# Kernel tuning notes

Hardware: AMD Instinct MI355X
Metric: run time of the kernel (lower is better)

## Reference

```python
import jax, jax.numpy as jnp
import numpy as np

N = 50000  # num nodes


def _gcn_layer(x, W, b, src, dst, dinv):
    # PyG GCNConv: transform first, then normalized neighbor aggregation
    h = x @ W                                   # [N, out]
    norm = dinv[src] * dinv[dst]                # [E]
    msg = h[src] * norm[:, None]                # gather + scale, [E, out]
    agg = jax.ops.segment_sum(msg, dst, num_segments=N)
    agg = agg + h * (dinv * dinv)[:, None]      # self-loop term (weight 1)
    return agg + b


def setup_inputs() -> dict:
    key = jax.random.key(0)
    ks = jax.random.split(key, 9)
    x = jax.random.normal(ks[0], (N, 256), dtype=jnp.float32)
    edge_index = jax.random.randint(ks[1], (2, 800000), 0, N, dtype=jnp.int64)
    def lin(kw, kb, fan_in, fan_out):
        s = 1.0 / np.sqrt(fan_in)
        W = jax.random.uniform(kw, (fan_in, fan_out), jnp.float32, -s, s)
        b = jax.random.uniform(kb, (fan_out,), jnp.float32, -s, s)
        return W, b
    W0, b0 = lin(ks[2], ks[3], 256, 128)
    W1, b1 = lin(ks[4], ks[5], 128, 128)
    W2, b2 = lin(ks[6], ks[7], 128, 64)
    return {"x": x, "edge_index": edge_index,
            "W0": W0, "b0": b0, "W1": W1, "b1": b1, "W2": W2, "b2": b2}


def reference(x, edge_index, W0, b0, W1, b1, W2, b2):
    src, dst = edge_index[0], edge_index[1]
    # degree with implicit self loops (edge weights = 1)
    deg = jax.ops.segment_sum(jnp.ones_like(dst, dtype=x.dtype), dst,
                              num_segments=N) + 1.0
    dinv = jax.lax.rsqrt(deg)
    h = jax.nn.relu(_gcn_layer(x, W0, b0, src, dst, dinv))
    h = jax.nn.relu(_gcn_layer(h, W1, b1, src, dst, dinv))
    out = _gcn_layer(h, W2, b2, src, dst, dinv)  # no relu on final layer
    return out
```

## Files before the change

### kernel.cpp

```cpp
#include <hip/hip_runtime.h>

#define NNODES 50000
#define NEDGES 800000
#define CHUNK 3125

typedef __attribute__((ext_vector_type(8))) short short8;
typedef __attribute__((ext_vector_type(4))) float floatx4;
typedef __attribute__((ext_vector_type(8))) _Float16 f16x8;

__device__ __forceinline__ void async16(const void* g, void* l) {
    __builtin_amdgcn_global_load_lds(
        (const __attribute__((address_space(1))) unsigned int*)g,
        (__attribute__((address_space(3))) unsigned int*)l, 16, 0, 0);
}

__device__ __forceinline__ void split_bf16(float v, short& hi, short& lo) {
    unsigned u = __float_as_uint(v);
    unsigned hu = u & 0xffff0000u;
    hi = (short)(hu >> 16);
    float r = v - __uint_as_float(hu);
    lo = (short)(__float_as_uint(r) >> 16);
}


#define PREP_WBLK 224
#define PREP_TOT  (PREP_WBLK + 256)

__global__ __launch_bounds__(256) void k_prep(
    const float* __restrict__ W0, short* __restrict__ W0h, short* __restrict__ W0l,
    const float* __restrict__ W1, short* __restrict__ W1h, short* __restrict__ W1l,
    const float* __restrict__ W2, short* __restrict__ W2h, short* __restrict__ W2l,
    const int* __restrict__ dst, int* __restrict__ hist2d) {
    int b = blockIdx.x, t = threadIdx.x;
    if (b < PREP_WBLK) {
        int id = b * 256 + t;
        const float* W; short *Wh, *Wl; int K, F;
        if (id < 32768) { W = W0; Wh = W0h; Wl = W0l; K = 256; F = 128; }
        else if (id < 49152) { id -= 32768; W = W1; Wh = W1h; Wl = W1l; K = 128; F = 128; }
        else if (id < 57344) { id -= 49152; W = W2; Wh = W2h; Wl = W2l; K = 128; F = 64; }
        else return;
        int f = id / K, k = id - f * K;
        short h, l;
        split_bf16(W[(size_t)k * F + f], h, l);
        Wh[id] = h;
        Wl[id] = l;
    } else {
        __shared__ int h[256];
        int bb = b - PREP_WBLK;
        h[t] = 0;
        __syncthreads();
        int e0 = bb * CHUNK;
#pragma unroll
        for (int k = 0; k < 13; k++) {
            int o = k * 256 + t;
            if (o < CHUNK) atomicAdd(&h[dst[e0 + o] >> 8], 1);
        }
        __syncthreads();
        hist2d[bb * 256 + t] = h[t];
    }
}

__global__ __launch_bounds__(256) void k_p2(const int* __restrict__ src,
                                            const int* __restrict__ dst,
                                            const int* __restrict__ hist2d,
                                            unsigned* __restrict__ buck) {
    __shared__ int ex[256], cur[256];
    int t = threadIdx.x, b = blockIdx.x;
    int tot = 0, pre = 0;
    for (int bb = 0; bb < 256; bb++) {
        int v = hist2d[bb * 256 + t];
        tot += v;
        pre += (bb < b) ? v : 0;
    }
    ex[t] = tot;
    __syncthreads();
    for (int o = 1; o < 256; o <<= 1) {
        int xx = (t >= o) ? ex[t - o] : 0;
        __syncthreads();
        ex[t] += xx;
        __syncthreads();
    }
    cur[t] = (ex[t] - tot) + pre;
    __syncthreads();
    int e0 = b * CHUNK;
#pragma unroll
    for (int k = 0; k < 13; k++) {
        int o = k * 256 + t;
        if (o < CHUNK) {
            int s = src[e0 + o], d = dst[e0 + o];
            int p = atomicAdd(&cur[d >> 8], 1);
            buck[p] = (unsigned)s | ((unsigned)(d & 255) << 16);
        }
    }
}

__global__ __launch_bounds__(256) void k_p3(const unsigned* __restrict__ buck,
                                            const int* __restrict__ hist2d,
                                            int* __restrict__ rowptr,
                                            float* __restrict__ dinv,
                                            int* __restrict__ ssrc) {
    __shared__ int ex[256], cur[256], h[256], sS0[1], sS[1];
    int t = threadIdx.x, b = blockIdx.x;
    int tot = 0;
    for (int bb = 0; bb < 256; bb++) tot += hist2d[bb * 256 + t];
    ex[t] = tot;
    __syncthreads();
    for (int o = 1; o < 256; o <<= 1) {
        int xx = (t >= o) ? ex[t - o] : 0;
        __syncthreads();
        ex[t] += xx;
        __syncthreads();
    }
    if (t == b) { sS0[0] = ex[t] - tot; sS[0] = tot; }
    h[t] = 0;
    __syncthreads();
    int s0 = sS0[0], S = sS[0];
    for (int i = t; i < S; i += 256)
        atomicAdd(&h[(buck[s0 + i] >> 16) & 255], 1);
    __syncthreads();
    int v = h[t];
    ex[t] = v;
    __syncthreads();
    for (int o = 1; o < 256; o <<= 1) {
        int xx = (t >= o) ? ex[t - o] : 0;
        __syncthreads();
        ex[t] += xx;
        __syncthreads();
    }
    int excl = ex[t] - v;
    int n = b * 256 + t;
    if (n < NNODES) {
        rowptr[n] = s0 + excl;
        dinv[n] = rsqrtf((float)v + 1.0f);
    }
    if (b == 0 && t == 0) rowptr[NNODES] = NEDGES;
    cur[t] = excl;
    __syncthreads();
    for (int i = t; i < S; i += 256) {
        unsigned pk = buck[s0 + i];
        int dl = (pk >> 16) & 255;
        int p = atomicAdd(&cur[dl], 1);
        ssrc[s0 + p] = (int)(pk & 0xFFFFu);
    }
}


__global__ __launch_bounds__(256) void k_gemm0(
    const float* __restrict__ x, const short* __restrict__ Bh,
    const short* __restrict__ Bl, const float* __restrict__ dinv,
    _Float16* __restrict__ g16) {
    __shared__ __align__(16) short sAh[64 * 64], sAl[64 * 64];
    __shared__ __align__(16) short sBh[128 * 64], sBl[128 * 64];
    const int t = threadIdx.x, lane = t & 63, w = t >> 6;
    const int row0 = blockIdx.x * 64;
    const int lr = lane >> 3, lz = lane & 7;
    const int swz = (lz ^ lr) * 8;
    const int fr = lane & 15, fq = lane >> 4;
    floatx4 acc[8] = {};
    const int ar = t >> 2, ac = t & 3;
    int garow = row0 + ar;
    if (garow >= NNODES) garow = NNODES - 1;
    const float* xrow = x + (size_t)garow * 256 + ac * 16;

    for (int k0 = 0; k0 < 256; k0 += 64) {
        const float4* xp = (const float4*)(xrow + k0);
        float4 f0 = xp[0], f1 = xp[1], f2 = xp[2], f3 = xp[3];
        float va[16] = {f0.x, f0.y, f0.z, f0.w, f1.x, f1.y, f1.z, f1.w,
                        f2.x, f2.y, f2.z, f2.w, f3.x, f3.y, f3.z, f3.w};
        short8 h0, h1, l0, l1;
#pragma unroll
        for (int j = 0; j < 8; j++) {
            short h, l;
            split_bf16(va[j], h, l);     h0[j] = h; l0[j] = l;
            split_bf16(va[8 + j], h, l); h1[j] = h; l1[j] = l;
        }
        int c0 = ac * 2;
        *(short8*)&sAh[ar * 64 + ((c0 ^ (ar & 7)) * 8)] = h0;
        *(short8*)&sAh[ar * 64 + (((c0 + 1) ^ (ar & 7)) * 8)] = h1;
        *(short8*)&sAl[ar * 64 + ((c0 ^ (ar & 7)) * 8)] = l0;
        *(short8*)&sAl[ar * 64 + (((c0 + 1) ^ (ar & 7)) * 8)] = l1;
#pragma unroll
        for (int jj = 0; jj < 4; jj++) {
            int j = w * 4 + jj;
            size_t go = (size_t)(j * 8 + lr) * 256 + k0 + swz;
            async16(&Bh[go], &sBh[j * 512 + lane * 8]);
            async16(&Bl[go], &sBl[j * 512 + lane * 8]);
        }
        __syncthreads();
#pragma unroll
        for (int ks = 0; ks < 2; ks++) {
            int R = w * 16 + fr;
            int ca = ((ks * 4 + fq) ^ (R & 7)) * 8;
            short8 ah = *(const short8*)&sAh[R * 64 + ca];
            short8 al = *(const short8*)&sAl[R * 64 + ca];
#pragma unroll
            for (int nt = 0; nt < 8; nt++) {
                int n = nt * 16 + fr;
                int cb = ((ks * 4 + fq) ^ (n & 7)) * 8;
                short8 bh = *(const short8*)&sBh[n * 64 + cb];
                short8 bl = *(const short8*)&sBl[n * 64 + cb];
                acc[nt] = __builtin_amdgcn_mfma_f32_16x16x32_bf16(ah, bh, acc[nt], 0, 0, 0);
                acc[nt] = __builtin_amdgcn_mfma_f32_16x16x32_bf16(ah, bl, acc[nt], 0, 0, 0);
                acc[nt] = __builtin_amdgcn_mfma_f32_16x16x32_bf16(al, bh, acc[nt], 0, 0, 0);
            }
        }
        __syncthreads();
    }
#pragma unroll
    for (int rr = 0; rr < 4; rr++) {
        int gw = row0 + w * 16 + fq * 4 + rr;
        if (gw < NNODES) {
            float dv = dinv[gw];
#pragma unroll
            for (int nt = 0; nt < 8; nt++)
                g16[(size_t)gw * 128 + nt * 16 + fr] =
                    (_Float16)(acc[nt][rr] * dv);
        }
    }
}


template <int BN>
__global__ __launch_bounds__(256) void k_fagg(
    const _Float16* __restrict__ gin,
    const int* __restrict__ ssrc,
    const int* __restrict__ rowptr,
    const float* __restrict__ dinv,
    const float* __restrict__ bias,
    const short* __restrict__ Bh, const short* __restrict__ Bl,
    _Float16* __restrict__ gout) {
    constexpr int BM = 32;
    constexpr int NT = BN / 32;
    __shared__ __align__(16) short sAh[2 * BM * 64], sAl[2 * BM * 64];
    __shared__ __align__(16) char uB[16384];

    const int t = threadIdx.x, lane = t & 63, w = t >> 6;
    const int row0 = blockIdx.x * BM;

    int (*sED)[64] = (int(*)[64])uB;
    const int ln = t >> 3;
    const int c8 = t & 7;
    const f16x8* gp = (const f16x8*)gin;

    int gr = row0 + ln;
    if (gr >= NNODES) gr = NNODES - 1;
    int e0 = rowptr[gr], e1 = rowptr[gr + 1];
    int deg = e1 - e0;
    int cnt = deg < 64 ? deg : 64;
    for (int i = c8; i < cnt; i += 8) sED[ln][i] = ssrc[e0 + i];
    __syncthreads();

    f16x8 svA = gp[(size_t)gr * 16 + c8];
    f16x8 svB = gp[(size_t)gr * 16 + c8 + 8];
    float aA0[8], aA1[8], aB0[8], aB1[8];
#pragma unroll
    for (int j = 0; j < 8; j++) {
        aA0[j] = (float)svA[j]; aA1[j] = 0.f;
        aB0[j] = (float)svB[j]; aB1[j] = 0.f;
    }
    int i = 0;
    for (; i + 4 <= cnt; i += 4) {
        int s0 = sED[ln][i],     s1 = sED[ln][i + 1];
        int s2 = sED[ln][i + 2], s3 = sED[ln][i + 3];
        f16x8 vA0 = gp[(size_t)s0 * 16 + c8];
        f16x8 vB0 = gp[(size_t)s0 * 16 + c8 + 8];
        f16x8 vA1 = gp[(size_t)s1 * 16 + c8];
        f16x8 vB1 = gp[(size_t)s1 * 16 + c8 + 8];
        f16x8 vA2 = gp[(size_t)s2 * 16 + c8];
        f16x8 vB2 = gp[(size_t)s2 * 16 + c8 + 8];
        f16x8 vA3 = gp[(size_t)s3 * 16 + c8];
        f16x8 vB3 = gp[(size_t)s3 * 16 + c8 + 8];
#pragma unroll
        for (int j = 0; j < 8; j++) {
            aA0[j] += (float)vA0[j] + (float)vA2[j];
            aA1[j] += (float)vA1[j] + (float)vA3[j];
            aB0[j] += (float)vB0[j] + (float)vB2[j];
            aB1[j] += (float)vB1[j] + (float)vB3[j];
        }
    }
    for (; i < cnt; i++) {
        int s = sED[ln][i];
        f16x8 vA = gp[(size_t)s * 16 + c8];
        f16x8 vB = gp[(size_t)s * 16 + c8 + 8];
#pragma unroll
        for (int j = 0; j < 8; j++) {
            aA0[j] += (float)vA[j];
            aB0[j] += (float)vB[j];
        }
    }
    for (int e = e0 + 64; e < e1; e++) {
        int s = ssrc[e];
        f16x8 vA = gp[(size_t)s * 16 + c8];
        f16x8 vB = gp[(size_t)s * 16 + c8 + 8];
#pragma unroll
        for (int j = 0; j < 8; j++) {
            aA0[j] += (float)vA[j];
            aB0[j] += (float)vB[j];
        }
    }

    {
        float dv = dinv[gr];
        short8 h8, l8;
#pragma unroll
        for (int j = 0; j < 8; j++) {
            float o = (aA0[j] + aA1[j]) * dv + bias[c8 * 8 + j];
            o = fmaxf(o, 0.f);
            short h, l;
            split_bf16(o, h, l);
            h8[j] = h; l8[j] = l;
        }
        int ao0 = ln * 64 + ((c8 ^ (ln & 7)) * 8);
        *(short8*)&sAh[ao0] = h8;
        *(short8*)&sAl[ao0] = l8;
#pragma unroll
        for (int j = 0; j < 8; j++) {
            float o = (aB0[j] + aB1[j]) * dv + bias[(c8 + 8) * 8 + j];
            o = fmaxf(o, 0.f);
            short h, l;
            split_bf16(o, h, l);
            h8[j] = h; l8[j] = l;
        }
        int ao1 = BM * 64 + ao0;
        *(short8*)&sAh[ao1] = h8;
        *(short8*)&sAl[ao1] = l8;
    }
    __syncthreads();

    const int fr = lane & 15, fq = lane >> 4;
    const int lr = lane >> 3, lz = lane & 7;
    const int swz = (lz ^ lr) * 8;
    const int wr = w >> 1, wc = w & 1;
    floatx4 acc[NT] = {};

    if constexpr (BN == 128) {
        short* sB = (short*)uB;
#pragma unroll
        for (int kt = 0; kt < 2; kt++) {
#pragma unroll
            for (int jj = 0; jj < 4; jj++) {
                int j = w * 4 + jj;
                size_t go = (size_t)(j * 8 + lr) * 128 + kt * 64 + swz;
                async16(&Bh[go], &sB[j * 512 + lane * 8]);
            }
            __syncthreads();
#pragma unroll
            for (int ks = 0; ks < 2; ks++) {
                int R = wr * 16 + fr;
                int ca = kt * (BM * 64) + R * 64 + (((ks * 4 + fq) ^ (R & 7)) * 8);
                short8 ah = *(const short8*)&sAh[ca];
                short8 al = *(const short8*)&sAl[ca];
#pragma unroll
                for (int nt = 0; nt < NT; nt++) {
                    int n = wc * (BN / 2) + nt * 16 + fr;
                    int cb = n * 64 + (((ks * 4 + fq) ^ (n & 7)) * 8);
                    short8 bh = *(const short8*)&sB[cb];
                    acc[nt] = __builtin_amdgcn_mfma_f32_16x16x32_bf16(ah, bh, acc[nt], 0, 0, 0);
                    acc[nt] = __builtin_amdgcn_mfma_f32_16x16x32_bf16(al, bh, acc[nt], 0, 0, 0);
                }
            }
            __syncthreads();
#pragma unroll
            for (int jj = 0; jj < 4; jj++) {
                int j = w * 4 + jj;
                size_t go = (size_t)(j * 8 + lr) * 128 + kt * 64 + swz;
                async16(&Bl[go], &sB[j * 512 + lane * 8]);
            }
            __syncthreads();
#pragma unroll
            for (int ks = 0; ks < 2; ks++) {
                int R = wr * 16 + fr;
                int ca = kt * (BM * 64) + R * 64 + (((ks * 4 + fq) ^ (R & 7)) * 8);
                short8 ah = *(const short8*)&sAh[ca];
#pragma unroll
                for (int nt = 0; nt < NT; nt++) {
                    int n = wc * (BN / 2) + nt * 16 + fr;
                    int cb = n * 64 + (((ks * 4 + fq) ^ (n & 7)) * 8);
                    short8 bl = *(const short8*)&sB[cb];
                    acc[nt] = __builtin_amdgcn_mfma_f32_16x16x32_bf16(ah, bl, acc[nt], 0, 0, 0);
                }
            }
            __syncthreads();
        }
    } else {
        short* sBh_ = (short*)uB;
        short* sBl_ = (short*)uB + 64 * 64;
#pragma unroll
        for (int kt = 0; kt < 2; kt++) {
#pragma unroll
            for (int jj = 0; jj < 2; jj++) {
                int j = w * 2 + jj;
                size_t go = (size_t)(j * 8 + lr) * 128 + kt * 64 + swz;
                async16(&Bh[go], &sBh_[j * 512 + lane * 8]);
                async16(&Bl[go], &sBl_[j * 512 + lane * 8]);
            }
            __syncthreads();
#pragma unroll
            for (int ks = 0; ks < 2; ks++) {
                int R = wr * 16 + fr;
                int ca = kt * (BM * 64) + R * 64 + (((ks * 4 + fq) ^ (R & 7)) * 8);
                short8 ah = *(const short8*)&sAh[ca];
                short8 al = *(const short8*)&sAl[ca];
#pragma unroll
                for (int nt = 0; nt < NT; nt++) {
                    int n = wc * (BN / 2) + nt * 16 + fr;
                    int cb = n * 64 + (((ks * 4 + fq) ^ (n & 7)) * 8);
                    short8 bh = *(const short8*)&sBh_[cb];
                    short8 bl = *(const short8*)&sBl_[cb];
                    acc[nt] = __builtin_amdgcn_mfma_f32_16x16x32_bf16(ah, bh, acc[nt], 0, 0, 0);
                    acc[nt] = __builtin_amdgcn_mfma_f32_16x16x32_bf16(ah, bl, acc[nt], 0, 0, 0);
                    acc[nt] = __builtin_amdgcn_mfma_f32_16x16x32_bf16(al, bh, acc[nt], 0, 0, 0);
                }
            }
            __syncthreads();
        }
    }

#pragma unroll
    for (int rr = 0; rr < 4; rr++) {
        int grow = row0 + wr * 16 + fq * 4 + rr;
        if (grow < NNODES) {
            float dv = dinv[grow];
#pragma unroll
            for (int nt = 0; nt < NT; nt++)
                gout[(size_t)grow * BN + wc * (BN / 2) + nt * 16 + fr] =
                    (_Float16)(acc[nt][rr] * dv);
        }
    }
}


__global__ __launch_bounds__(256) void k_agg64(const _Float16* __restrict__ g,
                                               const int* __restrict__ ssrc,
                                               const int* __restrict__ rowptr,
                                               const float* __restrict__ dinv,
                                               const float* __restrict__ bias,
                                               float* __restrict__ outf) {
    constexpr int NPB = 64;
    __shared__ int sED[NPB][64];
    int t = threadIdx.x;
    int ln = t >> 2;
    int c8 = t & 3;
    int n = blockIdx.x * NPB + ln;
    bool valid = (n < NNODES);
    int nc = valid ? n : NNODES - 1;

    int e0 = rowptr[nc], e1 = rowptr[nc + 1];
    int deg = e1 - e0;
    int cnt = deg < 64 ? deg : 64;
    for (int i = c8; i < cnt; i += 4) sED[ln][i] = ssrc[e0 + i];
    __syncthreads();

    const f16x8* gp = (const f16x8*)g;
    f16x8 svA = gp[(size_t)nc * 8 + c8];
    f16x8 svB = gp[(size_t)nc * 8 + c8 + 4];
    float aA0[8], aA1[8], aB0[8], aB1[8];
#pragma unroll
    for (int j = 0; j < 8; j++) {
        aA0[j] = (float)svA[j]; aA1[j] = 0.f;
        aB0[j] = (float)svB[j]; aB1[j] = 0.f;
    }
    int i = 0;
    for (; i + 4 <= cnt; i += 4) {
        int s0 = sED[ln][i],     s1 = sED[ln][i + 1];
        int s2 = sED[ln][i + 2], s3 = sED[ln][i + 3];
        f16x8 vA0 = gp[(size_t)s0 * 8 + c8];
        f16x8 vB0 = gp[(size_t)s0 * 8 + c8 + 4];
        f16x8 vA1 = gp[(size_t)s1 * 8 + c8];
        f16x8 vB1 = gp[(size_t)s1 * 8 + c8 + 4];
        f16x8 vA2 = gp[(size_t)s2 * 8 + c8];
        f16x8 vB2 = gp[(size_t)s2 * 8 + c8 + 4];
        f16x8 vA3 = gp[(size_t)s3 * 8 + c8];
        f16x8 vB3 = gp[(size_t)s3 * 8 + c8 + 4];
#pragma unroll
        for (int j = 0; j < 8; j++) {
            aA0[j] += (float)vA0[j] + (float)vA2[j];
            aA1[j] += (float)vA1[j] + (float)vA3[j];
            aB0[j] += (float)vB0[j] + (float)vB2[j];
            aB1[j] += (float)vB1[j] + (float)vB3[j];
        }
    }
    for (; i < cnt; i++) {
        int s = sED[ln][i];
        f16x8 vA = gp[(size_t)s * 8 + c8];
        f16x8 vB = gp[(size_t)s * 8 + c8 + 4];
#pragma unroll
        for (int j = 0; j < 8; j++) {
            aA0[j] += (float)vA[j];
            aB0[j] += (float)vB[j];
        }
    }
    for (int e = e0 + 64; e < e1; e++) {
        int s = ssrc[e];
        f16x8 vA = gp[(size_t)s * 8 + c8];
        f16x8 vB = gp[(size_t)s * 8 + c8 + 4];
#pragma unroll
        for (int j = 0; j < 8; j++) {
            aA0[j] += (float)vA[j];
            aB0[j] += (float)vB[j];
        }
    }

    if (!valid) return;
    float dv = dinv[nc];
    float oA[8], oB[8];
#pragma unroll
    for (int j = 0; j < 8; j++) {
        oA[j] = (aA0[j] + aA1[j]) * dv + bias[c8 * 8 + j];
        oB[j] = (aB0[j] + aB1[j]) * dv + bias[(c8 + 4) * 8 + j];
    }
    *(float4*)&outf[(size_t)n * 64 + c8 * 8] =
        make_float4(oA[0], oA[1], oA[2], oA[3]);
    *(float4*)&outf[(size_t)n * 64 + c8 * 8 + 4] =
        make_float4(oA[4], oA[5], oA[6], oA[7]);
    *(float4*)&outf[(size_t)n * 64 + (c8 + 4) * 8] =
        make_float4(oB[0], oB[1], oB[2], oB[3]);
    *(float4*)&outf[(size_t)n * 64 + (c8 + 4) * 8 + 4] =
        make_float4(oB[4], oB[5], oB[6], oB[7]);
}


static inline size_t align256(size_t x) { return (x + 255) & ~(size_t)255; }

extern "C" void kernel_launch(void* const* d_in, const int* in_sizes, int n_in,
                              void* d_out, int out_size, void* d_ws, size_t ws_size,
                              hipStream_t stream) {
    const float* x  = (const float*)d_in[0];
    const int*   ei = (const int*)d_in[1];
    const float* W0 = (const float*)d_in[2];
    const float* b0 = (const float*)d_in[3];
    const float* W1 = (const float*)d_in[4];
    const float* b1 = (const float*)d_in[5];
    const float* W2 = (const float*)d_in[6];
    const float* b2 = (const float*)d_in[7];
    float* out = (float*)d_out;

    const int* src = ei;
    const int* dst = ei + NEDGES;

    char* w = (char*)d_ws;
    size_t off = 0;
    float* dinv    = (float*)(w + off); off = align256(off + NNODES * 4);
    int* rowptr    = (int*)(w + off);   off = align256(off + (NNODES + 1) * 4);
    int* hist2d    = (int*)(w + off);   off = align256(off + 256 * 256 * 4);
    unsigned* buck = (unsigned*)(w + off); off = align256(off + (size_t)NEDGES * 4);
    int* ssrc      = (int*)(w + off);   off = align256(off + (size_t)NEDGES * 4);
    short* W0h     = (short*)(w + off); off = align256(off + 256 * 128 * 2);
    short* W0l     = (short*)(w + off); off = align256(off + 256 * 128 * 2);
    short* W1h     = (short*)(w + off); off = align256(off + 128 * 128 * 2);
    short* W1l     = (short*)(w + off); off = align256(off + 128 * 128 * 2);
    short* W2h     = (short*)(w + off); off = align256(off + 128 * 64 * 2);
    short* W2l     = (short*)(w + off); off = align256(off + 128 * 64 * 2);
    _Float16* g16a = (_Float16*)(w + off); off = align256(off + (size_t)NNODES * 128 * 2);
    _Float16* g16b = (_Float16*)(w + off); off = align256(off + (size_t)NNODES * 128 * 2);
    _Float16* g16c = (_Float16*)(w + off); off = align256(off + (size_t)NNODES * 64 * 2);

    const int MB = (NNODES + 63) / 64;
    const int FB = (NNODES + 31) / 32;
    const int AB = (NNODES + 63) / 64;

    k_prep<<<PREP_TOT, 256, 0, stream>>>(W0, W0h, W0l, W1, W1h, W1l,
                                         W2, W2h, W2l, dst, hist2d);
    k_p2<<<256, 256, 0, stream>>>(src, dst, hist2d, buck);
    k_p3<<<256, 256, 0, stream>>>(buck, hist2d, rowptr, dinv, ssrc);

    k_gemm0<<<MB, 256, 0, stream>>>(x, W0h, W0l, dinv, g16a);
    k_fagg<128><<<FB, 256, 0, stream>>>(g16a, ssrc, rowptr, dinv, b0,
                                        W1h, W1l, g16b);
    k_fagg<64><<<FB, 256, 0, stream>>>(g16b, ssrc, rowptr, dinv, b1,
                                       W2h, W2l, g16c);
    k_agg64<<<AB, 256, 0, stream>>>(g16c, ssrc, rowptr, dinv, b2, out);
    (void)in_sizes; (void)n_in; (void)out_size; (void)ws_size;
}
```

Baseline: 239.6 us.

## Merge first-layer GEMM into bucket-scatter kernel using atomic global degree counts

The prep kernel now also builds a per-node in-degree array with global atomics, so the layer-0 GEMM can compute its normalisation without waiting on the CSR build kernel. The GEMM blocks are appended to the bucket-scatter launch, letting the dense transform overlap the sort phase and removing one kernel launch. In exchange it adds 800k global atomics to prep, a memset launch, and extra LDS per block for the scatter-only blocks, which may reduce their occupancy.

Result: slower. 260.3 us (+8.6%).

```diff
diff --git a/kernel.cpp b/kernel.cpp
--- a/kernel.cpp
+++ b/kernel.cpp
@@ -30,7 +30,8 @@
     const float* __restrict__ W0, short* __restrict__ W0h, short* __restrict__ W0l,
     const float* __restrict__ W1, short* __restrict__ W1h, short* __restrict__ W1l,
     const float* __restrict__ W2, short* __restrict__ W2h, short* __restrict__ W2l,
-    const int* __restrict__ dst, int* __restrict__ hist2d) {
+    const int* __restrict__ dst, int* __restrict__ hist2d,
+    int* __restrict__ deg) {
     int b = blockIdx.x, t = threadIdx.x;
     if (b < PREP_WBLK) {
         int id = b * 256 + t;
@@ -53,43 +54,125 @@
 #pragma unroll
         for (int k = 0; k < 13; k++) {
             int o = k * 256 + t;
-            if (o < CHUNK) atomicAdd(&h[dst[e0 + o] >> 8], 1);
+            if (o < CHUNK) {
+                int d = dst[e0 + o];
+                atomicAdd(&h[d >> 8], 1);
+                atomicAdd(&deg[d], 1);
+            }
         }
         __syncthreads();
         hist2d[bb * 256 + t] = h[t];
     }
 }
 
-__global__ __launch_bounds__(256) void k_p2(const int* __restrict__ src,
-                                            const int* __restrict__ dst,
-                                            const int* __restrict__ hist2d,
-                                            unsigned* __restrict__ buck) {
+
+#define G0_MB ((NNODES + 63) / 64)
+
+__global__ __launch_bounds__(256) void k_p2g0(
+    const int* __restrict__ src, const int* __restrict__ dst,
+    const int* __restrict__ hist2d, unsigned* __restrict__ buck,
+    const float* __restrict__ x, const short* __restrict__ Bh,
+    const short* __restrict__ Bl, const int* __restrict__ deg,
+    _Float16* __restrict__ g16) {
+    __shared__ __align__(16) short sAh[64 * 64], sAl[64 * 64];
+    __shared__ __align__(16) short sBh[128 * 64], sBl[128 * 64];
     __shared__ int ex[256], cur[256];
-    int t = threadIdx.x, b = blockIdx.x;
-    int tot = 0, pre = 0;
-    for (int bb = 0; bb < 256; bb++) {
-        int v = hist2d[bb * 256 + t];
-        tot += v;
-        pre += (bb < b) ? v : 0;
-    }
-    ex[t] = tot;
-    __syncthreads();
-    for (int o = 1; o < 256; o <<= 1) {
-        int xx = (t >= o) ? ex[t - o] : 0;
-        __syncthreads();
-        ex[t] += xx;
-        __syncthreads();
-    }
-    cur[t] = (ex[t] - tot) + pre;
-    __syncthreads();
-    int e0 = b * CHUNK;
-#pragma unroll
-    for (int k = 0; k < 13; k++) {
-        int o = k * 256 + t;
-        if (o < CHUNK) {
-            int s = src[e0 + o], d = dst[e0 + o];
-            int p = atomicAdd(&cur[d >> 8], 1);
-            buck[p] = (unsigned)s | ((unsigned)(d & 255) << 16);
+
+    if (blockIdx.x < 256) {
+        int t = threadIdx.x, b = blockIdx.x;
+        int tot = 0, pre = 0;
+        for (int bb = 0; bb < 256; bb++) {
+            int v = hist2d[bb * 256 + t];
+            tot += v;
+            pre += (bb < b) ? v : 0;
+        }
+        ex[t] = tot;
+        __syncthreads();
+        for (int o = 1; o < 256; o <<= 1) {
+            int xx = (t >= o) ? ex[t - o] : 0;
+            __syncthreads();
+            ex[t] += xx;
+            __syncthreads();
+        }
+        cur[t] = (ex[t] - tot) + pre;
+        __syncthreads();
+        int e0 = b * CHUNK;
+#pragma unroll
+        for (int k = 0; k < 13; k++) {
+            int o = k * 256 + t;
+            if (o < CHUNK) {
+                int s = src[e0 + o], d = dst[e0 + o];
+                int p = atomicAdd(&cur[d >> 8], 1);
+                buck[p] = (unsigned)s | ((unsigned)(d & 255) << 16);
+            }
+        }
+        return;
+    }
+
+    const int t = threadIdx.x, lane = t & 63, w = t >> 6;
+    const int row0 = (blockIdx.x - 256) * 64;
+    const int lr = lane >> 3, lz = lane & 7;
+    const int swz = (lz ^ lr) * 8;
+    const int fr = lane & 15, fq = lane >> 4;
+    floatx4 acc[8] = {};
+    const int ar = t >> 2, ac = t & 3;
+    int garow = row0 + ar;
+    if (garow >= NNODES) garow = NNODES - 1;
+    const float* xrow = x + (size_t)garow * 256 + ac * 16;
+
+    for (int k0 = 0; k0 < 256; k0 += 64) {
+        const float4* xp = (const float4*)(xrow + k0);
+        float4 f0 = xp[0], f1 = xp[1], f2 = xp[2], f3 = xp[3];
+        float va[16] = {f0.x, f0.y, f0.z, f0.w, f1.x, f1.y, f1.z, f1.w,
+                        f2.x, f2.y, f2.z, f2.w, f3.x, f3.y, f3.z, f3.w};
+        short8 h0, h1, l0, l1;
+#pragma unroll
+        for (int j = 0; j < 8; j++) {
+            short h, l;
+            split_bf16(va[j], h, l);     h0[j] = h; l0[j] = l;
+            split_bf16(va[8 + j], h, l); h1[j] = h; l1[j] = l;
+        }
+        int c0 = ac * 2;
+        *(short8*)&sAh[ar * 64 + ((c0 ^ (ar & 7)) * 8)] = h0;
+        *(short8*)&sAh[ar * 64 + (((c0 + 1) ^ (ar & 7)) * 8)] = h1;
+        *(short8*)&sAl[ar * 64 + ((c0 ^ (ar & 7)) * 8)] = l0;
+        *(short8*)&sAl[ar * 64 + (((c0 + 1) ^ (ar & 7)) * 8)] = l1;
+#pragma unroll
+        for (int jj = 0; jj < 4; jj++) {
+            int j = w * 4 + jj;
+            size_t go = (size_t)(j * 8 + lr) * 256 + k0 + swz;
+            async16(&Bh[go], &sBh[j * 512 + lane * 8]);
+            async16(&Bl[go], &sBl[j * 512 + lane * 8]);
+        }
+        __syncthreads();
+#pragma unroll
+        for (int ks = 0; ks < 2; ks++) {
+            int R = w * 16 + fr;
+            int ca = ((ks * 4 + fq) ^ (R & 7)) * 8;
+            short8 ah = *(const short8*)&sAh[R * 64 + ca];
+            short8 al = *(const short8*)&sAl[R * 64 + ca];
+#pragma unroll
+            for (int nt = 0; nt < 8; nt++) {
+                int n = nt * 16 + fr;
+                int cb = ((ks * 4 + fq) ^ (n & 7)) * 8;
+                short8 bh = *(const short8*)&sBh[n * 64 + cb];
+                short8 bl = *(const short8*)&sBl[n * 64 + cb];
+                acc[nt] = __builtin_amdgcn_mfma_f32_16x16x32_bf16(ah, bh, acc[nt], 0, 0, 0);
+                acc[nt] = __builtin_amdgcn_mfma_f32_16x16x32_bf16(ah, bl, acc[nt], 0, 0, 0);
+                acc[nt] = __builtin_amdgcn_mfma_f32_16x16x32_bf16(al, bh, acc[nt], 0, 0, 0);
+            }
+        }
+        __syncthreads();
+    }
+#pragma unroll
+    for (int rr = 0; rr < 4; rr++) {
+        int gw = row0 + w * 16 + fq * 4 + rr;
+        if (gw < NNODES) {
+            float dv = rsqrtf((float)deg[gw] + 1.0f);
+#pragma unroll
+            for (int nt = 0; nt < 8; nt++)
+                g16[(size_t)gw * 128 + nt * 16 + fr] =
+                    (_Float16)(acc[nt][rr] * dv);
         }
     }
 }
@@ -141,81 +224,6 @@
         int dl = (pk >> 16) & 255;
         int p = atomicAdd(&cur[dl], 1);
         ssrc[s0 + p] = (int)(pk & 0xFFFFu);
-    }
-}
-
-
-__global__ __launch_bounds__(256) void k_gemm0(
-    const float* __restrict__ x, const short* __restrict__ Bh,
-    const short* __restrict__ Bl, const float* __restrict__ dinv,
-    _Float16* __restrict__ g16) {
-    __shared__ __align__(16) short sAh[64 * 64], sAl[64 * 64];
-    __shared__ __align__(16) short sBh[128 * 64], sBl[128 * 64];
-    const int t = threadIdx.x, lane = t & 63, w = t >> 6;
-    const int row0 = blockIdx.x * 64;
-    const int lr = lane >> 3, lz = lane & 7;
-    const int swz = (lz ^ lr) * 8;
-    const int fr = lane & 15, fq = lane >> 4;
-    floatx4 acc[8] = {};
-    const int ar = t >> 2, ac = t & 3;
-    int garow = row0 + ar;
-    if (garow >= NNODES) garow = NNODES - 1;
-    const float* xrow = x + (size_t)garow * 256 + ac * 16;
-
-    for (int k0 = 0; k0 < 256; k0 += 64) {
-        const float4* xp = (const float4*)(xrow + k0);
-        float4 f0 = xp[0], f1 = xp[1], f2 = xp[2], f3 = xp[3];
-        float va[16] = {f0.x, f0.y, f0.z, f0.w, f1.x, f1.y, f1.z, f1.w,
-                        f2.x, f2.y, f2.z, f2.w, f3.x, f3.y, f3.z, f3.w};
-        short8 h0, h1, l0, l1;
-#pragma unroll
-        for (int j = 0; j < 8; j++) {
-            short h, l;
-            split_bf16(va[j], h, l);     h0[j] = h; l0[j] = l;
-            split_bf16(va[8 + j], h, l); h1[j] = h; l1[j] = l;
-        }
-        int c0 = ac * 2;
-        *(short8*)&sAh[ar * 64 + ((c0 ^ (ar & 7)) * 8)] = h0;
-        *(short8*)&sAh[ar * 64 + (((c0 + 1) ^ (ar & 7)) * 8)] = h1;
-        *(short8*)&sAl[ar * 64 + ((c0 ^ (ar & 7)) * 8)] = l0;
-        *(short8*)&sAl[ar * 64 + (((c0 + 1) ^ (ar & 7)) * 8)] = l1;
-#pragma unroll
-        for (int jj = 0; jj < 4; jj++) {
-            int j = w * 4 + jj;
-            size_t go = (size_t)(j * 8 + lr) * 256 + k0 + swz;
-            async16(&Bh[go], &sBh[j * 512 + lane * 8]);
-            async16(&Bl[go], &sBl[j * 512 + lane * 8]);
-        }
-        __syncthreads();
-#pragma unroll
-        for (int ks = 0; ks < 2; ks++) {
-            int R = w * 16 + fr;
-            int ca = ((ks * 4 + fq) ^ (R & 7)) * 8;
-            short8 ah = *(const short8*)&sAh[R * 64 + ca];
-            short8 al = *(const short8*)&sAl[R * 64 + ca];
-#pragma unroll
-            for (int nt = 0; nt < 8; nt++) {
-                int n = nt * 16 + fr;
-                int cb = ((ks * 4 + fq) ^ (n & 7)) * 8;
-                short8 bh = *(const short8*)&sBh[n * 64 + cb];
-                short8 bl = *(const short8*)&sBl[n * 64 + cb];
-                acc[nt] = __builtin_amdgcn_mfma_f32_16x16x32_bf16(ah, bh, acc[nt], 0, 0, 0);
-                acc[nt] = __builtin_amdgcn_mfma_f32_16x16x32_bf16(ah, bl, acc[nt], 0, 0, 0);
-                acc[nt] = __builtin_amdgcn_mfma_f32_16x16x32_bf16(al, bh, acc[nt], 0, 0, 0);
-            }
-        }
-        __syncthreads();
-    }
-#pragma unroll
-    for (int rr = 0; rr < 4; rr++) {
-        int gw = row0 + w * 16 + fq * 4 + rr;
-        if (gw < NNODES) {
-            float dv = dinv[gw];
-#pragma unroll
-            for (int nt = 0; nt < 8; nt++)
-                g16[(size_t)gw * 128 + nt * 16 + fr] =
-                    (_Float16)(acc[nt][rr] * dv);
-        }
     }
 }
 
@@ -541,6 +549,7 @@
     char* w = (char*)d_ws;
     size_t off = 0;
     float* dinv    = (float*)(w + off); off = align256(off + NNODES * 4);
+    int* deg       = (int*)(w + off);   off = align256(off + NNODES * 4);
     int* rowptr    = (int*)(w + off);   off = align256(off + (NNODES + 1) * 4);
     int* hist2d    = (int*)(w + off);   off = align256(off + 256 * 256 * 4);
     unsigned* buck = (unsigned*)(w + off); off = align256(off + (size_t)NEDGES * 4);
@@ -555,16 +564,16 @@
     _Float16* g16b = (_Float16*)(w + off); off = align256(off + (size_t)NNODES * 128 * 2);
     _Float16* g16c = (_Float16*)(w + off); off = align256(off + (size_t)NNODES * 64 * 2);
 
-    const int MB = (NNODES + 63) / 64;
     const int FB = (NNODES + 31) / 32;
     const int AB = (NNODES + 63) / 64;
 
+    hipMemsetAsync(deg, 0, NNODES * sizeof(int), stream);
     k_prep<<<PREP_TOT, 256, 0, stream>>>(W0, W0h, W0l, W1, W1h, W1l,
-                                         W2, W2h, W2l, dst, hist2d);
-    k_p2<<<256, 256, 0, stream>>>(src, dst, hist2d, buck);
+                                         W2, W2h, W2l, dst, hist2d, deg);
+    k_p2g0<<<256 + G0_MB, 256, 0, stream>>>(src, dst, hist2d, buck,
+                                            x, W0h, W0l, deg, g16a);
     k_p3<<<256, 256, 0, stream>>>(buck, hist2d, rowptr, dinv, ssrc);
 
-    k_gemm0<<<MB, 256, 0, stream>>>(x, W0h, W0l, dinv, g16a);
     k_fagg<128><<<FB, 256, 0, stream>>>(g16a, ssrc, rowptr, dinv, b0,
                                         W1h, W1l, g16b);
     k_fagg<64><<<FB, 256, 0, stream>>>(g16b, ssrc, rowptr, dinv, b1,
```
